# Performance work log

Measured on AMD Instinct MI355X. Metric: run time of the kernel, lower is better.

## Reference

```python
import jax, jax.numpy as jnp
import numpy as np

NUM_CLASSES = 14
TAU = 1.0
LOSS_WEIGHT = 1.0
KERNEL_SUM = 26.0  # 3x3x3 ones with center zeroed


def setup_inputs() -> dict:
    key = jax.random.key(0)
    k1, k2, k3 = jax.random.split(key, 3)
    B, C, H, W, D = 2, NUM_CLASSES, 96, 96, 96
    preds_S = jax.random.normal(k1, (B, C, H, W, D), dtype=jnp.float32)
    preds_T = jax.random.normal(k2, (B, C, H, W, D), dtype=jnp.float32)
    gt_labels = jax.random.randint(k3, (B, 1, H, W, D), 0, NUM_CLASSES).astype(jnp.int32)
    return {"preds_S": preds_S, "preds_T": preds_T, "gt_labels": gt_labels}


def _boundary_masks(gt_labels, num_classes):
    # gt_labels: [B,1,H,W,D] int -> boundary mask [B,K,H,W,D] bool
    B, _, H, W, D = gt_labels.shape
    onehot = (gt_labels == jnp.arange(num_classes, dtype=gt_labels.dtype)[None, :, None, None, None]).astype(jnp.float32)  # [B,K,H,W,D]
    kernel = jnp.ones((1, 1, 3, 3, 3), jnp.float32).at[0, 0, 1, 1, 1].set(0.0)
    x = onehot.reshape(B * num_classes, 1, H, W, D)
    conv = jax.lax.conv_general_dilated(x, kernel, (1, 1, 1), 'SAME')  # [B*K,1,H,W,D]
    conv = conv.reshape(B, num_classes, H, W, D)
    # boundary[boundary == kernel.sum()] = 0; boundary[boundary > 0] = 1
    return (conv > 0.0) & (conv != KERNEL_SUM)


def reference(preds_S, preds_T, gt_labels):
    B, C, H, W, D = preds_S.shape
    V = H * W * D
    # softmax over class dim is per-voxel, identical before/after the gather
    logS = jax.nn.log_softmax(preds_S / TAU, axis=1).reshape(B, C, V)
    logT = jax.nn.log_softmax(preds_T / TAU, axis=1).reshape(B, C, V)
    pT = jnp.exp(logT)
    kl_per_voxel = jnp.sum(pT * (logT - logS), axis=1)  # [B,V] (sum over classes)

    mask = _boundary_masks(gt_labels, NUM_CLASSES).reshape(B, NUM_CLASSES, V).astype(jnp.float32)
    n_b = jnp.sum(mask, axis=-1)                                  # [B,K] boundary voxel counts
    masked_sum = jnp.einsum('bkv,bv->bk', mask, kl_per_voxel)     # [B,K]
    # F.kl_div reduction='mean' averages over all C * n_b elements
    per_cls = jnp.where(n_b > 0, masked_sum / (C * jnp.maximum(n_b, 1.0)), 0.0)
    valid = (n_b > 0).astype(jnp.float32)
    n_valid = jnp.sum(valid)
    loss = jnp.where(n_valid > 0, jnp.sum(per_cls) / jnp.maximum(n_valid, 1.0), 0.0)
    return LOSS_WEIGHT * loss
```

## Files before the change

kernel.cpp:

```cpp
#include <hip/hip_runtime.h>

#define NC 14
#define DIM 96
#define VOL (96 * 96 * 96)
#define VPT 4
#define TPB 256
#define VPB (VPT * TPB)
#define NBPB (VOL / VPB)

__global__ __launch_bounds__(256, 2) void bkd_main(const float* __restrict__ S,
                                                   const float* __restrict__ T,
                                                   const int* __restrict__ L,
                                                   float* __restrict__ partials) {
    const int b = blockIdx.x / NBPB;
    const int local = blockIdx.x % NBPB;
    const int tid = threadIdx.x;
    const int v0 = local * VPB + tid * VPT;
    const int d0 = v0 % DIM;
    const int w = (v0 / DIM) % DIM;
    const int h = v0 / (DIM * DIM);

    const float* Sb = S + (size_t)b * NC * VOL + v0;
    const float* Tb = T + (size_t)b * NC * VOL + v0;
    const int* lab = L + b * VOL;

    const bool has_lo = (d0 > 0);
    const bool has_hi = (d0 + VPT < DIM);
    int4 q[9];
    int plo[9], phi[9];
    bool cvalid[9];
#pragma unroll
    for (int dh = -1; dh <= 1; ++dh) {
#pragma unroll
        for (int dw = -1; dw <= 1; ++dw) {
            const int ci = (dh + 1) * 3 + (dw + 1);
            const int h2 = h + dh, w2 = w + dw;
            const bool ok = ((unsigned)h2 < DIM) & ((unsigned)w2 < DIM);
            cvalid[ci] = ok;
            const int* p = lab + (h2 * DIM + w2) * DIM + d0;
            if (ok) {
                q[ci] = *(const int4*)p;
                plo[ci] = has_lo ? p[-1] : 0;
                phi[ci] = has_hi ? p[4] : 0;
            }
        }
    }

    float4 sv[NC], tv[NC];
#pragma unroll
    for (int c = 0; c < NC; ++c) {
        sv[c] = *(const float4*)(Sb + c * VOL);
        tv[c] = *(const float4*)(Tb + c * VOL);
    }

    unsigned vmask[VPT] = {0u, 0u, 0u, 0u};
#pragma unroll
    for (int ci = 0; ci < 9; ++ci) {
        if (cvalid[ci]) {
            const unsigned m1 = 1u << q[ci].x;
            const unsigned m2 = 1u << q[ci].y;
            const unsigned m3 = 1u << q[ci].z;
            const unsigned m4 = 1u << q[ci].w;
            const unsigned m0 = has_lo ? (1u << plo[ci]) : 0u;
            const unsigned m5 = has_hi ? (1u << phi[ci]) : 0u;
            const bool isC = (ci == 4);
            vmask[0] |= m0 | m2 | (isC ? 0u : m1);
            vmask[1] |= m1 | m3 | (isC ? 0u : m2);
            vmask[2] |= m2 | m4 | (isC ? 0u : m3);
            vmask[3] |= m3 | m5 | (isC ? 0u : m4);
        }
    }
    {
        const int nh = 3 - (h == 0) - (h == DIM - 1);
        const int nw = 3 - (w == 0) - (w == DIM - 1);
        const int ncols = nh * nw;
        const int nn0 = ncols * (has_lo ? 3 : 2) - 1;
        const int nn12 = ncols * 3 - 1;
        const int nn3 = ncols * (has_hi ? 3 : 2) - 1;
        if (nn0 == 26 && __popc(vmask[0]) == 1) vmask[0] = 0u;
        if (nn12 == 26 && __popc(vmask[1]) == 1) vmask[1] = 0u;
        if (nn12 == 26 && __popc(vmask[2]) == 1) vmask[2] = 0u;
        if (nn3 == 26 && __popc(vmask[3]) == 1) vmask[3] = 0u;
    }

    float ES[VPT] = {0.f, 0.f, 0.f, 0.f};
    float ET[VPT] = {0.f, 0.f, 0.f, 0.f};
    float Aa[VPT] = {0.f, 0.f, 0.f, 0.f};
#pragma unroll
    for (int c = 0; c < NC; ++c) {
        const float4 s = sv[c];
        const float4 t = tv[c];
        { const float es = __expf(s.x), et = __expf(t.x);
          ES[0] += es; ET[0] += et; Aa[0] += et * (t.x - s.x); }
        { const float es = __expf(s.y), et = __expf(t.y);
          ES[1] += es; ET[1] += et; Aa[1] += et * (t.y - s.y); }
        { const float es = __expf(s.z), et = __expf(t.z);
          ES[2] += es; ET[2] += et; Aa[2] += et * (t.z - s.z); }
        { const float es = __expf(s.w), et = __expf(t.w);
          ES[3] += es; ET[3] += et; Aa[3] += et * (t.w - s.w); }
    }

    float kl[VPT];
#pragma unroll
    for (int i = 0; i < VPT; ++i) {
        kl[i] = Aa[i] / ET[i] + __logf(ES[i]) - __logf(ET[i]);
    }

    float acc_sum[NC];
    float acc_cnt[NC];
#pragma unroll
    for (int k = 0; k < NC; ++k) { acc_sum[k] = 0.f; acc_cnt[k] = 0.f; }
#pragma unroll
    for (int i = 0; i < VPT; ++i) {
#pragma unroll
        for (int k = 0; k < NC; ++k) {
            if (vmask[i] & (1u << k)) { acc_sum[k] += kl[i]; acc_cnt[k] += 1.f; }
        }
    }

    __shared__ float lds[4][2 * NC];
    const int lane = tid & 63, wid = tid >> 6;
#pragma unroll
    for (int k = 0; k < NC; ++k) {
        float svv = acc_sum[k], cvv = acc_cnt[k];
#pragma unroll
        for (int off = 32; off; off >>= 1) {
            svv += __shfl_xor(svv, off);
            cvv += __shfl_xor(cvv, off);
        }
        if (lane == 0) { lds[wid][k] = svv; lds[wid][NC + k] = cvv; }
    }
    __syncthreads();
    if (tid < 2 * NC) {
        const float r = lds[0][tid] + lds[1][tid] + lds[2][tid] + lds[3][tid];
        const int k = (tid < NC) ? tid : (tid - NC);
        const int p = (tid < NC) ? (b * NC + k) : (2 * NC + b * NC + k);
        partials[p * NBPB + local] = r;
    }
}

__global__ __launch_bounds__(64) void bkd_reduce(const float* __restrict__ partials,
                                                 float* __restrict__ res) {
    const int p = blockIdx.x;
    const int lane = threadIdx.x;
    float acc = 0.f;
    for (int i = lane; i < NBPB; i += 64) acc += partials[p * NBPB + i];
#pragma unroll
    for (int off = 32; off; off >>= 1) acc += __shfl_xor(acc, off);
    if (lane == 0) res[p] = acc;
}

__global__ __launch_bounds__(64) void bkd_last(const float* __restrict__ res,
                                               float* __restrict__ out) {
    const int j = threadIdx.x;
    float per = 0.f, valid = 0.f;
    if (j < 2 * NC) {
        const float nb = res[2 * NC + j];
        if (nb > 0.f) {
            per = res[j] / (NC * nb);
            valid = 1.f;
        }
    }
#pragma unroll
    for (int off = 32; off; off >>= 1) {
        per += __shfl_xor(per, off);
        valid += __shfl_xor(valid, off);
    }
    if (j == 0) out[0] = (valid > 0.f) ? (per / valid) : 0.f;
}

extern "C" void kernel_launch(void* const* d_in, const int* in_sizes, int n_in,
                              void* d_out, int out_size, void* d_ws, size_t ws_size,
                              hipStream_t stream) {
    const float* S = (const float*)d_in[0];
    const float* T = (const float*)d_in[1];
    const int* L = (const int*)d_in[2];
    float* out = (float*)d_out;
    float* partials = (float*)d_ws;
    float* res = partials + 2 * NC * 2 * NBPB;

    bkd_main<<<dim3(2 * NBPB), dim3(TPB), 0, stream>>>(S, T, L, partials);
    bkd_reduce<<<dim3(4 * NC), dim3(64), 0, stream>>>(partials, res);
    bkd_last<<<dim3(1), dim3(64), 0, stream>>>(res, out);
}
```

Baseline: 52.47 us.

## Process two voxel chunks per block and pack per-class counts into 16-bit lanes

Each block now loops over two consecutive 1024-voxel chunks, halving the grid size and the number of per-block partials. Per-class boundary counts are packed two per 32-bit word, which halves the count reductions (7 packed words instead of 14 floats). Launch bounds are raised to 4 waves per SIMD to raise occupancy. The goal is less reduction and partial-write overhead per voxel, at the risk of register pressure from the unrolled two-iteration loop and fewer blocks to hide latency.

Result: slower. 142.9 us (+172.4%).

```diff
diff --git a/kernel.cpp b/kernel.cpp
--- a/kernel.cpp
+++ b/kernel.cpp
@@ -6,136 +6,159 @@
 #define VPT 4
 #define TPB 256
 #define VPB (VPT * TPB)
-#define NBPB (VOL / VPB)
-
-__global__ __launch_bounds__(256, 2) void bkd_main(const float* __restrict__ S,
+#define NCHUNK (VOL / VPB)
+#define ITERS 2
+#define NBT (NCHUNK / ITERS)
+
+__global__ __launch_bounds__(256, 4) void bkd_main(const float* __restrict__ S,
                                                    const float* __restrict__ T,
                                                    const int* __restrict__ L,
                                                    float* __restrict__ partials) {
-    const int b = blockIdx.x / NBPB;
-    const int local = blockIdx.x % NBPB;
+    const int b = blockIdx.x / NBT;
+    const int local = blockIdx.x % NBT;
     const int tid = threadIdx.x;
-    const int v0 = local * VPB + tid * VPT;
-    const int d0 = v0 % DIM;
-    const int w = (v0 / DIM) % DIM;
-    const int h = v0 / (DIM * DIM);
-
-    const float* Sb = S + (size_t)b * NC * VOL + v0;
-    const float* Tb = T + (size_t)b * NC * VOL + v0;
+
+    const float* Sbase = S + (size_t)b * NC * VOL;
+    const float* Tbase = T + (size_t)b * NC * VOL;
     const int* lab = L + b * VOL;
 
-    const bool has_lo = (d0 > 0);
-    const bool has_hi = (d0 + VPT < DIM);
-    int4 q[9];
-    int plo[9], phi[9];
-    bool cvalid[9];
-#pragma unroll
-    for (int dh = -1; dh <= 1; ++dh) {
-#pragma unroll
-        for (int dw = -1; dw <= 1; ++dw) {
-            const int ci = (dh + 1) * 3 + (dw + 1);
-            const int h2 = h + dh, w2 = w + dw;
-            const bool ok = ((unsigned)h2 < DIM) & ((unsigned)w2 < DIM);
-            cvalid[ci] = ok;
-            const int* p = lab + (h2 * DIM + w2) * DIM + d0;
-            if (ok) {
-                q[ci] = *(const int4*)p;
-                plo[ci] = has_lo ? p[-1] : 0;
-                phi[ci] = has_hi ? p[4] : 0;
-            }
-        }
-    }
-
-    float4 sv[NC], tv[NC];
-#pragma unroll
-    for (int c = 0; c < NC; ++c) {
-        sv[c] = *(const float4*)(Sb + c * VOL);
-        tv[c] = *(const float4*)(Tb + c * VOL);
-    }
-
-    unsigned vmask[VPT] = {0u, 0u, 0u, 0u};
-#pragma unroll
-    for (int ci = 0; ci < 9; ++ci) {
-        if (cvalid[ci]) {
-            const unsigned m1 = 1u << q[ci].x;
-            const unsigned m2 = 1u << q[ci].y;
-            const unsigned m3 = 1u << q[ci].z;
-            const unsigned m4 = 1u << q[ci].w;
-            const unsigned m0 = has_lo ? (1u << plo[ci]) : 0u;
-            const unsigned m5 = has_hi ? (1u << phi[ci]) : 0u;
-            const bool isC = (ci == 4);
-            vmask[0] |= m0 | m2 | (isC ? 0u : m1);
-            vmask[1] |= m1 | m3 | (isC ? 0u : m2);
-            vmask[2] |= m2 | m4 | (isC ? 0u : m3);
-            vmask[3] |= m3 | m5 | (isC ? 0u : m4);
-        }
-    }
-    {
-        const int nh = 3 - (h == 0) - (h == DIM - 1);
-        const int nw = 3 - (w == 0) - (w == DIM - 1);
-        const int ncols = nh * nw;
-        const int nn0 = ncols * (has_lo ? 3 : 2) - 1;
-        const int nn12 = ncols * 3 - 1;
-        const int nn3 = ncols * (has_hi ? 3 : 2) - 1;
-        if (nn0 == 26 && __popc(vmask[0]) == 1) vmask[0] = 0u;
-        if (nn12 == 26 && __popc(vmask[1]) == 1) vmask[1] = 0u;
-        if (nn12 == 26 && __popc(vmask[2]) == 1) vmask[2] = 0u;
-        if (nn3 == 26 && __popc(vmask[3]) == 1) vmask[3] = 0u;
-    }
-
-    float ES[VPT] = {0.f, 0.f, 0.f, 0.f};
-    float ET[VPT] = {0.f, 0.f, 0.f, 0.f};
-    float Aa[VPT] = {0.f, 0.f, 0.f, 0.f};
-#pragma unroll
-    for (int c = 0; c < NC; ++c) {
-        const float4 s = sv[c];
-        const float4 t = tv[c];
-        { const float es = __expf(s.x), et = __expf(t.x);
-          ES[0] += es; ET[0] += et; Aa[0] += et * (t.x - s.x); }
-        { const float es = __expf(s.y), et = __expf(t.y);
-          ES[1] += es; ET[1] += et; Aa[1] += et * (t.y - s.y); }
-        { const float es = __expf(s.z), et = __expf(t.z);
-          ES[2] += es; ET[2] += et; Aa[2] += et * (t.z - s.z); }
-        { const float es = __expf(s.w), et = __expf(t.w);
-          ES[3] += es; ET[3] += et; Aa[3] += et * (t.w - s.w); }
-    }
-
-    float kl[VPT];
-#pragma unroll
-    for (int i = 0; i < VPT; ++i) {
-        kl[i] = Aa[i] / ET[i] + __logf(ES[i]) - __logf(ET[i]);
-    }
-
     float acc_sum[NC];
-    float acc_cnt[NC];
-#pragma unroll
-    for (int k = 0; k < NC; ++k) { acc_sum[k] = 0.f; acc_cnt[k] = 0.f; }
-#pragma unroll
-    for (int i = 0; i < VPT; ++i) {
-#pragma unroll
-        for (int k = 0; k < NC; ++k) {
-            if (vmask[i] & (1u << k)) { acc_sum[k] += kl[i]; acc_cnt[k] += 1.f; }
-        }
-    }
-
-    __shared__ float lds[4][2 * NC];
+    unsigned cntpk[7];
+#pragma unroll
+    for (int k = 0; k < NC; ++k) acc_sum[k] = 0.f;
+#pragma unroll
+    for (int j = 0; j < 7; ++j) cntpk[j] = 0u;
+
+#pragma unroll
+    for (int it = 0; it < ITERS; ++it) {
+        const int v0 = (ITERS * local + it) * VPB + tid * VPT;
+        const int d0 = v0 % DIM;
+        const int w = (v0 / DIM) % DIM;
+        const int h = v0 / (DIM * DIM);
+        const bool has_lo = (d0 > 0);
+        const bool has_hi = (d0 + VPT < DIM);
+
+        int4 q[9];
+        int plo[9], phi[9];
+        bool cvalid[9];
+#pragma unroll
+        for (int dh = -1; dh <= 1; ++dh) {
+#pragma unroll
+            for (int dw = -1; dw <= 1; ++dw) {
+                const int ci = (dh + 1) * 3 + (dw + 1);
+                const int h2 = h + dh, w2 = w + dw;
+                const bool ok = ((unsigned)h2 < DIM) & ((unsigned)w2 < DIM);
+                cvalid[ci] = ok;
+                const int* p = lab + (h2 * DIM + w2) * DIM + d0;
+                if (ok) {
+                    q[ci] = *(const int4*)p;
+                    plo[ci] = has_lo ? p[-1] : 0;
+                    phi[ci] = has_hi ? p[4] : 0;
+                }
+            }
+        }
+
+        const float* Sb = Sbase + v0;
+        const float* Tb = Tbase + v0;
+        float4 sv[NC], tv[NC];
+#pragma unroll
+        for (int c = 0; c < NC; ++c) {
+            sv[c] = *(const float4*)(Sb + c * VOL);
+            tv[c] = *(const float4*)(Tb + c * VOL);
+        }
+
+        unsigned vmask[VPT] = {0u, 0u, 0u, 0u};
+#pragma unroll
+        for (int ci = 0; ci < 9; ++ci) {
+            if (cvalid[ci]) {
+                const unsigned m1 = 1u << q[ci].x;
+                const unsigned m2 = 1u << q[ci].y;
+                const unsigned m3 = 1u << q[ci].z;
+                const unsigned m4 = 1u << q[ci].w;
+                const unsigned m0 = has_lo ? (1u << plo[ci]) : 0u;
+                const unsigned m5 = has_hi ? (1u << phi[ci]) : 0u;
+                const bool isC = (ci == 4);
+                vmask[0] |= m0 | m2 | (isC ? 0u : m1);
+                vmask[1] |= m1 | m3 | (isC ? 0u : m2);
+                vmask[2] |= m2 | m4 | (isC ? 0u : m3);
+                vmask[3] |= m3 | m5 | (isC ? 0u : m4);
+            }
+        }
+        {
+            const int nh = 3 - (h == 0) - (h == DIM - 1);
+            const int nw = 3 - (w == 0) - (w == DIM - 1);
+            const int ncols = nh * nw;
+            const int nn0 = ncols * (has_lo ? 3 : 2) - 1;
+            const int nn12 = ncols * 3 - 1;
+            const int nn3 = ncols * (has_hi ? 3 : 2) - 1;
+            if (nn0 == 26 && __popc(vmask[0]) == 1) vmask[0] = 0u;
+            if (nn12 == 26 && __popc(vmask[1]) == 1) vmask[1] = 0u;
+            if (nn12 == 26 && __popc(vmask[2]) == 1) vmask[2] = 0u;
+            if (nn3 == 26 && __popc(vmask[3]) == 1) vmask[3] = 0u;
+        }
+
+        float ES[VPT] = {0.f, 0.f, 0.f, 0.f};
+        float ET[VPT] = {0.f, 0.f, 0.f, 0.f};
+        float Aa[VPT] = {0.f, 0.f, 0.f, 0.f};
+#pragma unroll
+        for (int c = 0; c < NC; ++c) {
+            const float4 s = sv[c];
+            const float4 t = tv[c];
+            { const float es = __expf(s.x), et = __expf(t.x);
+              ES[0] += es; ET[0] += et; Aa[0] += et * (t.x - s.x); }
+            { const float es = __expf(s.y), et = __expf(t.y);
+              ES[1] += es; ET[1] += et; Aa[1] += et * (t.y - s.y); }
+            { const float es = __expf(s.z), et = __expf(t.z);
+              ES[2] += es; ET[2] += et; Aa[2] += et * (t.z - s.z); }
+            { const float es = __expf(s.w), et = __expf(t.w);
+              ES[3] += es; ET[3] += et; Aa[3] += et * (t.w - s.w); }
+        }
+
+#pragma unroll
+        for (int i = 0; i < VPT; ++i) {
+            const float kl = Aa[i] / ET[i] + __logf(ES[i]) - __logf(ET[i]);
+            const unsigned m = vmask[i];
+            const unsigned long long y =
+                (unsigned long long)m | ((unsigned long long)m << 15);
+#pragma unroll
+            for (int j = 0; j < 7; ++j) {
+                cntpk[j] += (unsigned)((y >> (2 * j)) & 0x00010001ull);
+            }
+#pragma unroll
+            for (int k = 0; k < NC; ++k) {
+                if (m & (1u << k)) acc_sum[k] += kl;
+            }
+        }
+    }
+
+    __shared__ float lds_sum[4][NC];
+    __shared__ unsigned lds_cnt[4][7];
     const int lane = tid & 63, wid = tid >> 6;
 #pragma unroll
     for (int k = 0; k < NC; ++k) {
-        float svv = acc_sum[k], cvv = acc_cnt[k];
-#pragma unroll
-        for (int off = 32; off; off >>= 1) {
-            svv += __shfl_xor(svv, off);
-            cvv += __shfl_xor(cvv, off);
-        }
-        if (lane == 0) { lds[wid][k] = svv; lds[wid][NC + k] = cvv; }
+        float sv = acc_sum[k];
+#pragma unroll
+        for (int off = 32; off; off >>= 1) sv += __shfl_xor(sv, off);
+        if (lane == 0) lds_sum[wid][k] = sv;
+    }
+#pragma unroll
+    for (int j = 0; j < 7; ++j) {
+        unsigned cv = cntpk[j];
+#pragma unroll
+        for (int off = 32; off; off >>= 1) cv += (unsigned)__shfl_xor((int)cv, off);
+        if (lane == 0) lds_cnt[wid][j] = cv;
     }
     __syncthreads();
-    if (tid < 2 * NC) {
-        const float r = lds[0][tid] + lds[1][tid] + lds[2][tid] + lds[3][tid];
-        const int k = (tid < NC) ? tid : (tid - NC);
-        const int p = (tid < NC) ? (b * NC + k) : (2 * NC + b * NC + k);
-        partials[p * NBPB + local] = r;
+    if (tid < NC) {
+        const float r = lds_sum[0][tid] + lds_sum[1][tid] + lds_sum[2][tid] + lds_sum[3][tid];
+        partials[(b * NC + tid) * NBT + local] = r;
+    } else if (tid < 2 * NC) {
+        const int k = tid - NC;
+        unsigned c = 0;
+#pragma unroll
+        for (int w = 0; w < 4; ++w)
+            c += (lds_cnt[w][k >> 1] >> ((k & 1) * 16)) & 0xffffu;
+        partials[(2 * NC + b * NC + k) * NBT + local] = (float)c;
     }
 }
 
@@ -144,7 +167,7 @@
     const int p = blockIdx.x;
     const int lane = threadIdx.x;
     float acc = 0.f;
-    for (int i = lane; i < NBPB; i += 64) acc += partials[p * NBPB + i];
+    for (int i = lane; i < NBT; i += 64) acc += partials[p * NBT + i];
 #pragma unroll
     for (int off = 32; off; off >>= 1) acc += __shfl_xor(acc, off);
     if (lane == 0) res[p] = acc;
@@ -177,9 +200,9 @@
     const int* L = (const int*)d_in[2];
     float* out = (float*)d_out;
     float* partials = (float*)d_ws;
-    float* res = partials + 2 * NC * 2 * NBPB;
-
-    bkd_main<<<dim3(2 * NBPB), dim3(TPB), 0, stream>>>(S, T, L, partials);
+    float* res = partials + 4 * NC * NBT;
+
+    bkd_main<<<dim3(2 * NBT), dim3(TPB), 0, stream>>>(S, T, L, partials);
     bkd_reduce<<<dim3(4 * NC), dim3(64), 0, stream>>>(partials, res);
     bkd_last<<<dim3(1), dim3(64), 0, stream>>>(res, out);
 }
```
